# Performance work log

Hardware: AMD Instinct MI355X
Metric: run time of the kernel (lower is better)

The kernel has to match this reference:

```python
import jax, jax.numpy as jnp
import numpy as np

N = 50000   # nodes
E = 800000  # edges (avg degree 16)
F = 128     # n_input
H = 8       # n_heads
C = 16      # n_hidden (per-head out channels)
D = H * C   # 128


def setup_inputs() -> dict:
    key = jax.random.key(0)
    ks = jax.random.split(key, 12)
    s = lambda k, shape: (jax.random.normal(k, shape, dtype=jnp.float32) * 0.05)
    return {
        'x': jax.random.normal(ks[0], (N, F), dtype=jnp.float32),
        'edge_index': jax.random.randint(ks[1], (2, E), 0, N, dtype=jnp.int32),
        # GATv2Conv params (PyG defaults: share_weights=False, bias=True, neg_slope=0.2, self-loops)
        'W_l': s(ks[2], (F, D)),
        'b_l': jnp.zeros((D,), jnp.float32),
        'W_r': s(ks[3], (F, D)),
        'b_r': jnp.zeros((D,), jnp.float32),
        'att': s(ks[4], (H, C)),
        'conv_bias': jnp.zeros((D,), jnp.float32),
        # BatchNorm1d affine params
        'bn_gamma': jnp.ones((D,), jnp.float32),
        'bn_beta': jnp.zeros((D,), jnp.float32),
        # encoder output Linear
        'lin_W': s(ks[5], (D, D)),
        'lin_b': jnp.zeros((D,), jnp.float32),
        # EdgeDecoder scalars a, b (init 1.0)
        'a_edge': jnp.ones((1,), jnp.float32),
        'b_edge': jnp.ones((1,), jnp.float32),
        # LinearDecoder
        'dec2_W': s(ks[6], (D, F)),
        'dec2_b': jnp.zeros((F,), jnp.float32),
    }


def reference(x, edge_index, W_l, b_l, W_r, b_r, att, conv_bias,
              bn_gamma, bn_beta, lin_W, lin_b, a_edge, b_edge, dec2_W, dec2_b):
    n = x.shape[0]
    # GATv2Conv adds self-loops by default
    loop = jnp.arange(n, dtype=edge_index.dtype)
    src = jnp.concatenate([edge_index[0], loop])  # source j (messages come from)
    dst = jnp.concatenate([edge_index[1], loop])  # target i (softmax segments)
    xl = (x @ W_l + b_l).reshape(n, H, C)  # source transform
    xr = (x @ W_r + b_r).reshape(n, H, C)  # target transform
    # attention logits: a^T LeakyReLU(xl_j + xr_i), per head
    e = jax.nn.leaky_relu(xl[src] + xr[dst], negative_slope=0.2)  # [Et,H,C]
    logits = jnp.einsum('ehc,hc->eh', e, att)                     # [Et,H]
    # segment softmax over incoming edges of each target node
    m = jax.ops.segment_max(logits, dst, num_segments=n)
    ex = jnp.exp(logits - m[dst])
    denom = jax.ops.segment_sum(ex, dst, num_segments=n)
    alpha = ex / (denom[dst] + 1e-16)                             # [Et,H]
    # scatter-sum weighted source features, concat heads, add bias
    out = jax.ops.segment_sum(alpha[:, :, None] * xl[src], dst, num_segments=n)
    Hfeat = jax.nn.relu(out.reshape(n, D) + conv_bias)
    # BatchNorm1d, training-mode batch statistics (biased var), eps=1e-5
    mean = Hfeat.mean(axis=0)
    var = Hfeat.var(axis=0)
    Hn = (Hfeat - mean) / jnp.sqrt(var + 1e-5) * bn_gamma + bn_beta
    z = Hn @ lin_W + lin_b                                        # [N,D]
    # EdgeDecoder: gather + squared-diff + reduce over original edges
    dist = jnp.sum((z[edge_index[0]] - z[edge_index[1]]) ** 2, axis=1)  # [E]
    dist = jax.nn.relu(a_edge) * dist + b_edge
    value1 = jax.nn.sigmoid(-dist)                                # [E]
    # LinearDecoder
    value2 = z @ dec2_W + dec2_b                                  # [N,F]
    return (z, value1, value2)
```

## Files before the change

kernel.cpp:

```cpp
#include <hip/hip_runtime.h>

#define DD 128
#define HH 8
#define NBCOPY 32
#define PADS 4

typedef float f32x4 __attribute__((ext_vector_type(4)));
typedef short s16x8 __attribute__((ext_vector_type(8)));

__device__ __forceinline__ ushort f2b(float f) {
  unsigned u = __float_as_uint(f);
  unsigned r = u + 0x7fffu + ((u >> 16) & 1u);
  return (ushort)(r >> 16);
}
__device__ __forceinline__ float b2f(ushort b) {
  return __uint_as_float(((unsigned)b) << 16);
}
__device__ __forceinline__ void atomAddF(float* p, float v) {
#if defined(__HIP_DEVICE_COMPILE__)
  unsafeAtomicAdd(p, v);
#else
  atomicAdd(p, v);
#endif
}
__device__ __forceinline__ float lrelu(float v) { return fmaxf(v, 0.2f * v); }

__device__ __forceinline__ float sumC(const float* __restrict__ b8, int idx) {
  float s = 0.f;
#pragma unroll
  for (int c = 0; c < NBCOPY; c++) s += b8[(c << 8) + idx];
  return s;
}

__device__ __forceinline__ void packW_idx(int i, int& k, int& n) {
  int j = i & 7, l = (i >> 3) & 63, tile = i >> 9;
  int q = tile >> 3, c = tile & 7;
  k = q * 32 + ((l >> 4) << 3) + j;
  n = c * 16 + (l & 15);
}

__global__ __launch_bounds__(256) void k_prep(const float* __restrict__ x,
    ushort* __restrict__ xb, int total4, const float* __restrict__ Wl,
    const float* __restrict__ Wr, ushort* __restrict__ WlP,
    ushort* __restrict__ WrP, const int* __restrict__ ei,
    int* __restrict__ deg, int E, int convB, int packB) {
  int b = blockIdx.x;
  if (b < convB) {
    int i = b * 256 + threadIdx.x;
    if (i < total4) {
      float4 v = ((const float4*)x)[i];
      ushort4 o;
      o.x = f2b(v.x); o.y = f2b(v.y); o.z = f2b(v.z); o.w = f2b(v.w);
      ((ushort4*)xb)[i] = o;
    }
  } else if (b < convB + packB) {
    int t = (b - convB) * 256 + threadIdx.x;
    int side = t >> 14;
    int i = t & 16383;
    int k, n;
    packW_idx(i, k, n);
    if (side) WrP[i] = f2b(Wr[k * DD + n]);
    else      WlP[i] = f2b(Wl[k * DD + n]);
  } else {
    int e = (b - convB - packB) * 256 + threadIdx.x;
    if (e < E) atomicAdd(&deg[ei[E + e] << PADS], 1);
  }
}

__global__ __launch_bounds__(256) void k_part(const int* __restrict__ deg,
    int* __restrict__ rowstart, int* __restrict__ bsum, int N) {
  __shared__ int sc[256];
  int t = threadIdx.x;
  int i = blockIdx.x * 256 + t;
  int v = (i < N) ? deg[i << PADS] : 0;
  sc[t] = v;
  __syncthreads();
  for (int off = 1; off < 256; off <<= 1) {
    int u = (t >= off) ? sc[t - off] : 0;
    __syncthreads();
    sc[t] += u;
    __syncthreads();
  }
  if (i < N) rowstart[i] = sc[t] - v;
  if (t == 255) bsum[blockIdx.x] = sc[255];
}

__global__ __launch_bounds__(1024) void k_mid(const int* __restrict__ bsum,
    int* __restrict__ boff, int* __restrict__ rowstartN, int B) {
  __shared__ int sc[1024];
  int t = threadIdx.x;
  int v = (t < B) ? bsum[t] : 0;
  sc[t] = v;
  __syncthreads();
  for (int off = 1; off < 1024; off <<= 1) {
    int u = (t >= off) ? sc[t - off] : 0;
    __syncthreads();
    sc[t] += u;
    __syncthreads();
  }
  if (t < B) boff[t] = sc[t] - v;
  if (t == 1023) *rowstartN = sc[1023];
}

__global__ __launch_bounds__(256) void k_apply(int* __restrict__ rowstart,
    int* __restrict__ cursor, const int* __restrict__ boff, int N) {
  int i = blockIdx.x * 256 + threadIdx.x;
  if (i < N) {
    int r = rowstart[i] + boff[blockIdx.x];
    rowstart[i] = r;
    cursor[i << PADS] = r;
  }
}

__global__ __launch_bounds__(256) void k_lrfill(const ushort* __restrict__ xb,
    const ushort* __restrict__ WlP, const ushort* __restrict__ WrP,
    const float* __restrict__ bl, const float* __restrict__ br,
    ushort* __restrict__ xlb, ushort* __restrict__ xrb, int N, int mmB,
    const int* __restrict__ ei, int* __restrict__ cursor,
    int* __restrict__ csr_src, int E) {
  if ((int)blockIdx.x >= mmB) {
    int e = ((int)blockIdx.x - mmB) * 256 + threadIdx.x;
    if (e < E) {
      int d = ei[E + e];
      int pos = atomicAdd(&cursor[d << PADS], 1);
      csr_src[pos] = ei[e];
    }
    return;
  }
  int lane = threadIdx.x & 63;
  int wv = threadIdx.x >> 6;
  int rbase = blockIdx.x * 64 + wv * 16;
  int arow = rbase + (lane & 15);
  if (arow >= N) arow = 0;
  const ushort* ap = xb + (size_t)arow * DD + ((lane >> 4) << 3);
  s16x8 afr[4];
#pragma unroll
  for (int q = 0; q < 4; q++) afr[q] = *(const s16x8*)(ap + q * 32);
  const s16x8* BL = (const s16x8*)WlP;
  const s16x8* BR = (const s16x8*)WrP;
  f32x4 accL[8] = {}, accR[8] = {};
#pragma unroll
  for (int q = 0; q < 4; q++) {
#pragma unroll
    for (int c = 0; c < 8; c++) {
      accL[c] = __builtin_amdgcn_mfma_f32_16x16x32_bf16(
          afr[q], BL[(q * 8 + c) * 64 + lane], accL[c], 0, 0, 0);
      accR[c] = __builtin_amdgcn_mfma_f32_16x16x32_bf16(
          afr[q], BR[(q * 8 + c) * 64 + lane], accR[c], 0, 0, 0);
    }
  }
  int r0 = rbase + ((lane >> 4) << 2);
  int colb = lane & 15;
#pragma unroll
  for (int c = 0; c < 8; c++) {
    int col = c * 16 + colb;
    float vbl = bl[col], vbr = br[col];
#pragma unroll
    for (int r = 0; r < 4; r++) {
      int row = r0 + r;
      if (row < N) {
        xlb[(size_t)row * DD + col] = f2b(accL[c][r] + vbl);
        xrb[(size_t)row * DD + col] = f2b(accR[c][r] + vbr);
      }
    }
  }
}

__global__ __launch_bounds__(256) void k_agg(const ushort* __restrict__ xlb,
    const ushort* __restrict__ xrb, const int* __restrict__ rowstart,
    const int* __restrict__ csr_src, const float* __restrict__ att,
    const float* __restrict__ cb, ushort* __restrict__ hfb,
    float* __restrict__ bnsumC, int N) {
  int lane = threadIdx.x & 63;
  int wv = threadIdx.x >> 6;
  int d = (blockIdx.x * 256 + threadIdx.x) >> 6;
  bool active = d < N;
  int dc = active ? d : 0;
  float2 a = ((const float2*)att)[lane];
  float2 c = ((const float2*)cb)[lane];
  float vx = 0.f, vy = 0.f;
  {
    ushort2 rv = ((const ushort2*)(xrb + (size_t)dc * DD))[lane];
    float2 r = {b2f(rv.x), b2f(rv.y)};
    ushort2 gv = ((const ushort2*)(xlb + (size_t)dc * DD))[lane];
    float2 g0 = {b2f(gv.x), b2f(gv.y)};
    float t0 = lrelu(g0.x + r.x) * a.x + lrelu(g0.y + r.y) * a.y;
#pragma unroll
    for (int o = 4; o; o >>= 1) t0 += __shfl_xor(t0, o);
    float m0 = t0;
    float den0 = 1.f, den1 = 0.f, den2 = 0.f, den3 = 0.f;
    float2 acc0 = g0, acc1 = {0.f, 0.f}, acc2 = {0.f, 0.f}, acc3 = {0.f, 0.f};
    int i0 = rowstart[dc], i1 = active ? rowstart[dc + 1] : i0;
    int i = i0;
    for (; i + 4 <= i1; i += 4) {
      int s0 = csr_src[i], s1 = csr_src[i + 1];
      int s2 = csr_src[i + 2], s3 = csr_src[i + 3];
      ushort2 va = ((const ushort2*)(xlb + (size_t)s0 * DD))[lane];
      ushort2 vb = ((const ushort2*)(xlb + (size_t)s1 * DD))[lane];
      ushort2 vc = ((const ushort2*)(xlb + (size_t)s2 * DD))[lane];
      ushort2 vd = ((const ushort2*)(xlb + (size_t)s3 * DD))[lane];
      float2 ga = {b2f(va.x), b2f(va.y)};
      float2 gb = {b2f(vb.x), b2f(vb.y)};
      float2 gc = {b2f(vc.x), b2f(vc.y)};
      float2 gd = {b2f(vd.x), b2f(vd.y)};
      float ta = lrelu(ga.x + r.x) * a.x + lrelu(ga.y + r.y) * a.y;
      float tb = lrelu(gb.x + r.x) * a.x + lrelu(gb.y + r.y) * a.y;
      float tc = lrelu(gc.x + r.x) * a.x + lrelu(gc.y + r.y) * a.y;
      float td = lrelu(gd.x + r.x) * a.x + lrelu(gd.y + r.y) * a.y;
#pragma unroll
      for (int o = 4; o; o >>= 1) {
        ta += __shfl_xor(ta, o);
        tb += __shfl_xor(tb, o);
        tc += __shfl_xor(tc, o);
        td += __shfl_xor(td, o);
      }
      float ea = __expf(fminf(ta - m0, 60.f));
      float eb = __expf(fminf(tb - m0, 60.f));
      float ec = __expf(fminf(tc - m0, 60.f));
      float ed = __expf(fminf(td - m0, 60.f));
      den0 += ea; acc0.x += ea * ga.x; acc0.y += ea * ga.y;
      den1 += eb; acc1.x += eb * gb.x; acc1.y += eb * gb.y;
      den2 += ec; acc2.x += ec * gc.x; acc2.y += ec * gc.y;
      den3 += ed; acc3.x += ed * gd.x; acc3.y += ed * gd.y;
    }
    for (; i < i1; i++) {
      int s = csr_src[i];
      ushort2 va = ((const ushort2*)(xlb + (size_t)s * DD))[lane];
      float2 ga = {b2f(va.x), b2f(va.y)};
      float ta = lrelu(ga.x + r.x) * a.x + lrelu(ga.y + r.y) * a.y;
#pragma unroll
      for (int o = 4; o; o >>= 1) ta += __shfl_xor(ta, o);
      float ea = __expf(fminf(ta - m0, 60.f));
      den0 += ea;
      acc0.x += ea * ga.x;
      acc0.y += ea * ga.y;
    }
    float den = ((den0 + den1) + (den2 + den3)) + 1e-16f;
    float ax = (acc0.x + acc1.x) + (acc2.x + acc3.x);
    float ay = (acc0.y + acc1.y) + (acc2.y + acc3.y);
    float inv = 1.f / den;
    if (active) {
      vx = fmaxf(fmaf(ax, inv, c.x), 0.f);
      vy = fmaxf(fmaf(ay, inv, c.y), 0.f);
      ushort2 o2;
      o2.x = f2b(vx);
      o2.y = f2b(vy);
      ((ushort2*)(hfb + (size_t)dc * DD))[lane] = o2;
    }
  }
  __shared__ float4 red[4][64];
  red[wv][lane] = make_float4(vx, vx * vx, vy, vy * vy);
  __syncthreads();
  if (wv == 0) {
    float4 p0 = red[0][lane], p1 = red[1][lane];
    float4 p2 = red[2][lane], p3 = red[3][lane];
    float* bs = bnsumC + ((blockIdx.x & (NBCOPY - 1)) << 8);
    atomAddF(&bs[2 * lane],           (p0.x + p1.x) + (p2.x + p3.x));
    atomAddF(&bs[2 * lane + 1],       (p0.z + p1.z) + (p2.z + p3.z));
    atomAddF(&bs[DD + 2 * lane],      (p0.y + p1.y) + (p2.y + p3.y));
    atomAddF(&bs[DD + 2 * lane + 1],  (p0.w + p1.w) + (p2.w + p3.w));
  }
}

__global__ __launch_bounds__(256) void k_fold(const float* __restrict__ bnsumC,
    const float* __restrict__ gamma, const float* __restrict__ beta,
    const float* __restrict__ linW, const float* __restrict__ linb,
    const float* __restrict__ dec2W, const float* __restrict__ dec2b,
    float* __restrict__ b1p, float* __restrict__ b2pp,
    ushort* __restrict__ W1P, ushort* __restrict__ W2P, int N) {
  int b = blockIdx.x;
  float invN = 1.f / (float)N;
  if (b == 0) {
    int t = threadIdx.x;
    __shared__ float sshift[DD], sb1[DD];
    if (t < DD) {
      float mean = sumC(bnsumC, t) * invN;
      float var = sumC(bnsumC, DD + t) * invN - mean * mean;
      float sc = gamma[t] / sqrtf(var + 1e-5f);
      sshift[t] = beta[t] - mean * sc;
    }
    __syncthreads();
    if (t < DD) {
      float b1 = linb[t];
#pragma unroll 8
      for (int k = 0; k < DD; k++) b1 += sshift[k] * linW[k * DD + t];
      b1p[t] = b1;
      sb1[t] = b1;
    }
    __syncthreads();
    if (t < DD) {
      float b2v = dec2b[t];
#pragma unroll 8
      for (int k = 0; k < DD; k++) b2v += sb1[k] * dec2W[k * DD + t];
      b2pp[t] = b2v;
    }
  } else if (b <= 64) {
    int i = (b - 1) * 256 + threadIdx.x;
    int k, n;
    packW_idx(i, k, n);
    float mean = sumC(bnsumC, k) * invN;
    float var = sumC(bnsumC, DD + k) * invN - mean * mean;
    float sc = gamma[k] / sqrtf(var + 1e-5f);
    float s = 0.f;
#pragma unroll 8
    for (int kk = 0; kk < DD; kk++) s += linW[k * DD + kk] * dec2W[kk * DD + n];
    W2P[i] = f2b(sc * s);
  } else {
    int i = (b - 65) * 256 + threadIdx.x;
    int k, n;
    packW_idx(i, k, n);
    float mean = sumC(bnsumC, k) * invN;
    float var = sumC(bnsumC, DD + k) * invN - mean * mean;
    float sc = gamma[k] / sqrtf(var + 1e-5f);
    W1P[i] = f2b(sc * linW[k * DD + n]);
  }
}

__global__ __launch_bounds__(256) void k_mmz1(const ushort* __restrict__ hfb,
    const ushort* __restrict__ W1P, const float* __restrict__ b1p,
    float* __restrict__ z, ushort* __restrict__ zb, int N) {
  int lane = threadIdx.x & 63;
  int wv = threadIdx.x >> 6;
  int rbase = blockIdx.x * 64 + wv * 16;
  int arow = rbase + (lane & 15);
  if (arow >= N) arow = 0;
  const ushort* ap = hfb + (size_t)arow * DD + ((lane >> 4) << 3);
  s16x8 afr[4];
#pragma unroll
  for (int q = 0; q < 4; q++) afr[q] = *(const s16x8*)(ap + q * 32);
  const s16x8* B1 = (const s16x8*)W1P;
  f32x4 acc1[8] = {};
#pragma unroll
  for (int q = 0; q < 4; q++) {
#pragma unroll
    for (int c = 0; c < 8; c++) {
      acc1[c] = __builtin_amdgcn_mfma_f32_16x16x32_bf16(
          afr[q], B1[(q * 8 + c) * 64 + lane], acc1[c], 0, 0, 0);
    }
  }
  int r0 = rbase + ((lane >> 4) << 2);
  int colb = lane & 15;
#pragma unroll
  for (int c = 0; c < 8; c++) {
    int col = c * 16 + colb;
    float vb1 = b1p[col];
#pragma unroll
    for (int r = 0; r < 4; r++) {
      int row = r0 + r;
      if (row < N) {
        float zv = acc1[c][r] + vb1;
        z[(size_t)row * DD + col] = zv;
        zb[(size_t)row * DD + col] = f2b(zv);
      }
    }
  }
}

__global__ __launch_bounds__(256) void k_v2edge(const ushort* __restrict__ hfb,
    const ushort* __restrict__ W2P, const float* __restrict__ b2pp,
    float* __restrict__ v2, int N, int v2B,
    const ushort* __restrict__ zb, const int* __restrict__ ei,
    const float* __restrict__ ae, const float* __restrict__ be,
    float* __restrict__ v1, int E, int edgeB) {
  if ((int)blockIdx.x < v2B) {
    int lane = threadIdx.x & 63;
    int wv = threadIdx.x >> 6;
    int rbase = blockIdx.x * 64 + wv * 16;
    int arow = rbase + (lane & 15);
    if (arow >= N) arow = 0;
    const ushort* ap = hfb + (size_t)arow * DD + ((lane >> 4) << 3);
    s16x8 afr[4];
#pragma unroll
    for (int q = 0; q < 4; q++) afr[q] = *(const s16x8*)(ap + q * 32);
    const s16x8* B2 = (const s16x8*)W2P;
    f32x4 acc2[8] = {};
#pragma unroll
    for (int q = 0; q < 4; q++) {
#pragma unroll
      for (int c = 0; c < 8; c++) {
        acc2[c] = __builtin_amdgcn_mfma_f32_16x16x32_bf16(
            afr[q], B2[(q * 8 + c) * 64 + lane], acc2[c], 0, 0, 0);
      }
    }
    int r0 = rbase + ((lane >> 4) << 2);
    int colb = lane & 15;
#pragma unroll
    for (int c = 0; c < 8; c++) {
      int col = c * 16 + colb;
      float vb2 = b2pp[col];
#pragma unroll
      for (int r = 0; r < 4; r++) {
        int row = r0 + r;
        if (row < N) v2[(size_t)row * DD + col] = acc2[c][r] + vb2;
      }
    }
    return;
  }
  int lane = threadIdx.x & 63;
  int sub = lane >> 4;
  int cl = lane & 15;
  int wid = (((int)blockIdx.x - v2B) * 256 + threadIdx.x) >> 6;
  int nw = (edgeB * 256) >> 6;
  int nq = (E + 3) >> 2;
  float a = fmaxf(ae[0], 0.f), b = be[0];
  for (int q = wid; q < nq; q += nw) {
    int e = q * 4 + sub;
    bool ok = e < E;
    int ec = ok ? e : 0;
    int s = ei[ec], d = ei[E + ec];
    uint4 zs = *(const uint4*)(zb + (size_t)s * DD + cl * 8);
    uint4 zd = *(const uint4*)(zb + (size_t)d * DD + cl * 8);
    float v = 0.f;
    float dl, dh;
    dl = __uint_as_float(zs.x << 16) - __uint_as_float(zd.x << 16);
    dh = __uint_as_float(zs.x & 0xffff0000u) - __uint_as_float(zd.x & 0xffff0000u);
    v += dl * dl + dh * dh;
    dl = __uint_as_float(zs.y << 16) - __uint_as_float(zd.y << 16);
    dh = __uint_as_float(zs.y & 0xffff0000u) - __uint_as_float(zd.y & 0xffff0000u);
    v += dl * dl + dh * dh;
    dl = __uint_as_float(zs.z << 16) - __uint_as_float(zd.z << 16);
    dh = __uint_as_float(zs.z & 0xffff0000u) - __uint_as_float(zd.z & 0xffff0000u);
    v += dl * dl + dh * dh;
    dl = __uint_as_float(zs.w << 16) - __uint_as_float(zd.w << 16);
    dh = __uint_as_float(zs.w & 0xffff0000u) - __uint_as_float(zd.w & 0xffff0000u);
    v += dl * dl + dh * dh;
#pragma unroll
    for (int o = 8; o; o >>= 1) v += __shfl_xor(v, o);
    if (cl == 0 && ok) v1[e] = 1.f / (1.f + __expf(fmaf(a, v, b)));
  }
}

extern "C" void kernel_launch(void* const* d_in, const int* in_sizes, int n_in,
                              void* d_out, int out_size, void* d_ws, size_t ws_size,
                              hipStream_t stream) {
  const float* x = (const float*)d_in[0];
  const int* ei = (const int*)d_in[1];
  const float* Wl = (const float*)d_in[2];
  const float* bl = (const float*)d_in[3];
  const float* Wr = (const float*)d_in[4];
  const float* br = (const float*)d_in[5];
  const float* att = (const float*)d_in[6];
  const float* cb = (const float*)d_in[7];
  const float* gamma = (const float*)d_in[8];
  const float* beta = (const float*)d_in[9];
  const float* linW = (const float*)d_in[10];
  const float* linb = (const float*)d_in[11];
  const float* ae = (const float*)d_in[12];
  const float* be = (const float*)d_in[13];
  const float* dec2W = (const float*)d_in[14];
  const float* dec2b = (const float*)d_in[15];

  int N = in_sizes[0] / DD;
  int E = in_sizes[1] / 2;
  size_t ND = (size_t)N * DD;
  int B = (N + 255) / 256;

  char* wsb = (char*)d_ws;
  size_t o = 0;
  auto alloc = [&](size_t bytes) {
    void* p = wsb + o;
    o += (bytes + 15) & ~(size_t)15;
    return p;
  };
  ushort* xb  = (ushort*)alloc(ND * 2);
  ushort* xlb = (ushort*)alloc(ND * 2);
  ushort* xrb = (ushort*)alloc(ND * 2);
  ushort* hfb = (ushort*)alloc(ND * 2);
  ushort* zbb = (ushort*)alloc(ND * 2);
  ushort* WlP = (ushort*)alloc(DD * DD * 2);
  ushort* WrP = (ushort*)alloc(DD * DD * 2);
  ushort* W1P = (ushort*)alloc(DD * DD * 2);
  ushort* W2P = (ushort*)alloc(DD * DD * 2);
  float* b1p   = (float*)alloc(DD * 4);
  float* b2pp  = (float*)alloc(DD * 4);
  int* deg       = (int*)alloc(((size_t)N << PADS) * 4 + 64);
  float* bnsumC  = (float*)alloc(NBCOPY * 2 * DD * 4);
  size_t clearBytes = (char*)(bnsumC + NBCOPY * 2 * DD) - (char*)deg;
  int* rowstart = (int*)alloc((size_t)(N + 1) * 4);
  int* cursor   = (int*)alloc(((size_t)N << PADS) * 4 + 64);
  int* bsum     = (int*)alloc((size_t)B * 4);
  int* boff     = (int*)alloc((size_t)B * 4);
  int* csr_src  = (int*)alloc((size_t)E * 4);

  float* z = (float*)d_out;
  float* v1 = z + ND;
  float* v2 = v1 + E;

  hipMemsetAsync(deg, 0, clearBytes, stream);

  int total4 = (int)(ND / 4);
  int convB = (total4 + 255) / 256;
  int packB = 128;
  int degB = (E + 255) / 256;
  k_prep<<<convB + packB + degB, 256, 0, stream>>>(x, xb, total4, Wl, Wr, WlP,
                                                   WrP, ei, deg, E, convB, packB);
  k_part<<<B, 256, 0, stream>>>(deg, rowstart, bsum, N);
  k_mid<<<1, 1024, 0, stream>>>(bsum, boff, rowstart + N, B);
  k_apply<<<B, 256, 0, stream>>>(rowstart, cursor, boff, N);
  int mmB = (N + 63) / 64;
  int fillB = (E + 255) / 256;
  k_lrfill<<<mmB + fillB, 256, 0, stream>>>(xb, WlP, WrP, bl, br, xlb, xrb, N,
                                            mmB, ei, cursor, csr_src, E);
  k_agg<<<(N + 3) / 4, 256, 0, stream>>>(xlb, xrb, rowstart, csr_src, att, cb,
                                         hfb, bnsumC, N);
  k_fold<<<129, 256, 0, stream>>>(bnsumC, gamma, beta, linW, linb, dec2W,
                                  dec2b, b1p, b2pp, W1P, W2P, N);
  k_mmz1<<<(N + 63) / 64, 256, 0, stream>>>(hfb, W1P, b1p, z, zbb, N);
  int v2B = (N + 63) / 64;
  int edgeB = 2048;
  k_v2edge<<<v2B + edgeB, 256, 0, stream>>>(hfb, W2P, b2pp, v2, N, v2B, zbb,
                                            ei, ae, be, v1, E, edgeB);
}
```

Measured before the change: 241.9 us.

## Compute edge decoder per destination node via CSR, reusing destination z row

The edge decoder now walks the existing CSR (grouped by destination) with one wavefront per node. Each wave loads the destination z row once and reuses it for all incoming edges, so only source rows are gathered per edge. To scatter results back to the original edge order, the CSR fill also writes an edge-id array, which costs an extra E-sized write and read. Output writes to v1 become scattered, and load balance now follows node degree.

```diff
diff --git a/kernel.cpp b/kernel.cpp
--- a/kernel.cpp
+++ b/kernel.cpp
@@ -117,13 +117,14 @@
     const float* __restrict__ bl, const float* __restrict__ br,
     ushort* __restrict__ xlb, ushort* __restrict__ xrb, int N, int mmB,
     const int* __restrict__ ei, int* __restrict__ cursor,
-    int* __restrict__ csr_src, int E) {
+    int* __restrict__ csr_src, int* __restrict__ csr_eid, int E) {
   if ((int)blockIdx.x >= mmB) {
     int e = ((int)blockIdx.x - mmB) * 256 + threadIdx.x;
     if (e < E) {
       int d = ei[E + e];
       int pos = atomicAdd(&cursor[d << PADS], 1);
       csr_src[pos] = ei[e];
+      csr_eid[pos] = e;
     }
     return;
   }
@@ -359,9 +360,10 @@
 __global__ __launch_bounds__(256) void k_v2edge(const ushort* __restrict__ hfb,
     const ushort* __restrict__ W2P, const float* __restrict__ b2pp,
     float* __restrict__ v2, int N, int v2B,
-    const ushort* __restrict__ zb, const int* __restrict__ ei,
+    const ushort* __restrict__ zb, const int* __restrict__ rowstart,
+    const int* __restrict__ csr_src, const int* __restrict__ csr_eid,
     const float* __restrict__ ae, const float* __restrict__ be,
-    float* __restrict__ v1, int E, int edgeB) {
+    float* __restrict__ v1) {
   if ((int)blockIdx.x < v2B) {
     int lane = threadIdx.x & 63;
     int wv = threadIdx.x >> 6;
@@ -399,34 +401,38 @@
   int lane = threadIdx.x & 63;
   int sub = lane >> 4;
   int cl = lane & 15;
-  int wid = (((int)blockIdx.x - v2B) * 256 + threadIdx.x) >> 6;
-  int nw = (edgeB * 256) >> 6;
-  int nq = (E + 3) >> 2;
+  int d = ((((int)blockIdx.x - v2B) * 256) + threadIdx.x) >> 6;
+  if (d >= N) return;
   float a = fmaxf(ae[0], 0.f), b = be[0];
-  for (int q = wid; q < nq; q += nw) {
-    int e = q * 4 + sub;
-    bool ok = e < E;
-    int ec = ok ? e : 0;
-    int s = ei[ec], d = ei[E + ec];
+  uint4 zdv = *(const uint4*)(zb + (size_t)d * DD + cl * 8);
+  float dz0 = __uint_as_float(zdv.x << 16);
+  float dz1 = __uint_as_float(zdv.x & 0xffff0000u);
+  float dz2 = __uint_as_float(zdv.y << 16);
+  float dz3 = __uint_as_float(zdv.y & 0xffff0000u);
+  float dz4 = __uint_as_float(zdv.z << 16);
+  float dz5 = __uint_as_float(zdv.z & 0xffff0000u);
+  float dz6 = __uint_as_float(zdv.w << 16);
+  float dz7 = __uint_as_float(zdv.w & 0xffff0000u);
+  int i0 = rowstart[d], i1 = rowstart[d + 1];
+  for (int i = i0; i < i1; i += 4) {
+    int idx = i + sub;
+    bool ok = idx < i1;
+    int ic = ok ? idx : i0;
+    int s = csr_src[ic];
+    int eid = csr_eid[ic];
     uint4 zs = *(const uint4*)(zb + (size_t)s * DD + cl * 8);
-    uint4 zd = *(const uint4*)(zb + (size_t)d * DD + cl * 8);
-    float v = 0.f;
-    float dl, dh;
-    dl = __uint_as_float(zs.x << 16) - __uint_as_float(zd.x << 16);
-    dh = __uint_as_float(zs.x & 0xffff0000u) - __uint_as_float(zd.x & 0xffff0000u);
-    v += dl * dl + dh * dh;
-    dl = __uint_as_float(zs.y << 16) - __uint_as_float(zd.y << 16);
-    dh = __uint_as_float(zs.y & 0xffff0000u) - __uint_as_float(zd.y & 0xffff0000u);
-    v += dl * dl + dh * dh;
-    dl = __uint_as_float(zs.z << 16) - __uint_as_float(zd.z << 16);
-    dh = __uint_as_float(zs.z & 0xffff0000u) - __uint_as_float(zd.z & 0xffff0000u);
-    v += dl * dl + dh * dh;
-    dl = __uint_as_float(zs.w << 16) - __uint_as_float(zd.w << 16);
-    dh = __uint_as_float(zs.w & 0xffff0000u) - __uint_as_float(zd.w & 0xffff0000u);
-    v += dl * dl + dh * dh;
+    float t, v;
+    t = __uint_as_float(zs.x << 16) - dz0;          v  = t * t;
+    t = __uint_as_float(zs.x & 0xffff0000u) - dz1;  v += t * t;
+    t = __uint_as_float(zs.y << 16) - dz2;          v += t * t;
+    t = __uint_as_float(zs.y & 0xffff0000u) - dz3;  v += t * t;
+    t = __uint_as_float(zs.z << 16) - dz4;          v += t * t;
+    t = __uint_as_float(zs.z & 0xffff0000u) - dz5;  v += t * t;
+    t = __uint_as_float(zs.w << 16) - dz6;          v += t * t;
+    t = __uint_as_float(zs.w & 0xffff0000u) - dz7;  v += t * t;
 #pragma unroll
     for (int o = 8; o; o >>= 1) v += __shfl_xor(v, o);
-    if (cl == 0 && ok) v1[e] = 1.f / (1.f + __expf(fmaf(a, v, b)));
+    if (cl == 0 && ok) v1[eid] = 1.f / (1.f + __expf(fmaf(a, v, b)));
   }
 }
 
@@ -481,6 +487,7 @@
   int* bsum     = (int*)alloc((size_t)B * 4);
   int* boff     = (int*)alloc((size_t)B * 4);
   int* csr_src  = (int*)alloc((size_t)E * 4);
+  int* csr_eid  = (int*)alloc((size_t)E * 4);
 
   float* z = (float*)d_out;
   float* v1 = z + ND;
@@ -500,14 +507,15 @@
   int mmB = (N + 63) / 64;
   int fillB = (E + 255) / 256;
   k_lrfill<<<mmB + fillB, 256, 0, stream>>>(xb, WlP, WrP, bl, br, xlb, xrb, N,
-                                            mmB, ei, cursor, csr_src, E);
+                                            mmB, ei, cursor, csr_src, csr_eid, E);
   k_agg<<<(N + 3) / 4, 256, 0, stream>>>(xlb, xrb, rowstart, csr_src, att, cb,
                                          hfb, bnsumC, N);
   k_fold<<<129, 256, 0, stream>>>(bnsumC, gamma, beta, linW, linb, dec2W,
                                   dec2b, b1p, b2pp, W1P, W2P, N);
   k_mmz1<<<(N + 63) / 64, 256, 0, stream>>>(hfb, W1P, b1p, z, zbb, N);
   int v2B = (N + 63) / 64;
-  int edgeB = 2048;
+  int edgeB = (N + 3) / 4;
   k_v2edge<<<v2B + edgeB, 256, 0, stream>>>(hfb, W2P, b2pp, v2, N, v2B, zbb,
-                                            ei, ae, be, v1, E, edgeB);
-}
+                                            rowstart, csr_src, csr_eid, ae, be,
+                                            v1);
+}
```

Result: slower. 260.4 us (+7.6%).

## Process decoder edges in CSR (dst-sorted) order and remap results back

Applied to the files above, without the earlier changes.

The CSR fill now stores (src,dst) pairs and records each edge's CSR position. The edge decoder walks edges in dst-sorted order, so the z[dst] gathers hit consecutive rows and get cache reuse. A new remap kernel then scatters the per-edge sigmoid values back to their original order. This costs an extra kernel launch, wider CSR entries in the aggregation loads, and extra E-sized buffers for writing and reading.

```diff
diff --git a/kernel.cpp b/kernel.cpp
--- a/kernel.cpp
+++ b/kernel.cpp
@@ -117,13 +117,14 @@
     const float* __restrict__ bl, const float* __restrict__ br,
     ushort* __restrict__ xlb, ushort* __restrict__ xrb, int N, int mmB,
     const int* __restrict__ ei, int* __restrict__ cursor,
-    int* __restrict__ csr_src, int E) {
+    int2* __restrict__ csr_sd, int* __restrict__ pose, int E) {
   if ((int)blockIdx.x >= mmB) {
     int e = ((int)blockIdx.x - mmB) * 256 + threadIdx.x;
     if (e < E) {
       int d = ei[E + e];
       int pos = atomicAdd(&cursor[d << PADS], 1);
-      csr_src[pos] = ei[e];
+      csr_sd[pos] = make_int2(ei[e], d);
+      pose[e] = pos;
     }
     return;
   }
@@ -168,7 +169,7 @@
 
 __global__ __launch_bounds__(256) void k_agg(const ushort* __restrict__ xlb,
     const ushort* __restrict__ xrb, const int* __restrict__ rowstart,
-    const int* __restrict__ csr_src, const float* __restrict__ att,
+    const int2* __restrict__ csr_sd, const float* __restrict__ att,
     const float* __restrict__ cb, ushort* __restrict__ hfb,
     float* __restrict__ bnsumC, int N) {
   int lane = threadIdx.x & 63;
@@ -193,12 +194,12 @@
     int i0 = rowstart[dc], i1 = active ? rowstart[dc + 1] : i0;
     int i = i0;
     for (; i + 4 <= i1; i += 4) {
-      int s0 = csr_src[i], s1 = csr_src[i + 1];
-      int s2 = csr_src[i + 2], s3 = csr_src[i + 3];
-      ushort2 va = ((const ushort2*)(xlb + (size_t)s0 * DD))[lane];
-      ushort2 vb = ((const ushort2*)(xlb + (size_t)s1 * DD))[lane];
-      ushort2 vc = ((const ushort2*)(xlb + (size_t)s2 * DD))[lane];
-      ushort2 vd = ((const ushort2*)(xlb + (size_t)s3 * DD))[lane];
+      int2 sd0 = csr_sd[i], sd1 = csr_sd[i + 1];
+      int2 sd2 = csr_sd[i + 2], sd3 = csr_sd[i + 3];
+      ushort2 va = ((const ushort2*)(xlb + (size_t)sd0.x * DD))[lane];
+      ushort2 vb = ((const ushort2*)(xlb + (size_t)sd1.x * DD))[lane];
+      ushort2 vc = ((const ushort2*)(xlb + (size_t)sd2.x * DD))[lane];
+      ushort2 vd = ((const ushort2*)(xlb + (size_t)sd3.x * DD))[lane];
       float2 ga = {b2f(va.x), b2f(va.y)};
       float2 gb = {b2f(vb.x), b2f(vb.y)};
       float2 gc = {b2f(vc.x), b2f(vc.y)};
@@ -224,7 +225,7 @@
       den3 += ed; acc3.x += ed * gd.x; acc3.y += ed * gd.y;
     }
     for (; i < i1; i++) {
-      int s = csr_src[i];
+      int s = csr_sd[i].x;
       ushort2 va = ((const ushort2*)(xlb + (size_t)s * DD))[lane];
       float2 ga = {b2f(va.x), b2f(va.y)};
       float ta = lrelu(ga.x + r.x) * a.x + lrelu(ga.y + r.y) * a.y;
@@ -359,9 +360,9 @@
 __global__ __launch_bounds__(256) void k_v2edge(const ushort* __restrict__ hfb,
     const ushort* __restrict__ W2P, const float* __restrict__ b2pp,
     float* __restrict__ v2, int N, int v2B,
-    const ushort* __restrict__ zb, const int* __restrict__ ei,
+    const ushort* __restrict__ zb, const int2* __restrict__ csr_sd,
     const float* __restrict__ ae, const float* __restrict__ be,
-    float* __restrict__ v1, int E, int edgeB) {
+    float* __restrict__ v1c, int E, int edgeB) {
   if ((int)blockIdx.x < v2B) {
     int lane = threadIdx.x & 63;
     int wv = threadIdx.x >> 6;
@@ -404,30 +405,31 @@
   int nq = (E + 3) >> 2;
   float a = fmaxf(ae[0], 0.f), b = be[0];
   for (int q = wid; q < nq; q += nw) {
-    int e = q * 4 + sub;
-    bool ok = e < E;
-    int ec = ok ? e : 0;
-    int s = ei[ec], d = ei[E + ec];
-    uint4 zs = *(const uint4*)(zb + (size_t)s * DD + cl * 8);
-    uint4 zd = *(const uint4*)(zb + (size_t)d * DD + cl * 8);
-    float v = 0.f;
-    float dl, dh;
-    dl = __uint_as_float(zs.x << 16) - __uint_as_float(zd.x << 16);
-    dh = __uint_as_float(zs.x & 0xffff0000u) - __uint_as_float(zd.x & 0xffff0000u);
-    v += dl * dl + dh * dh;
-    dl = __uint_as_float(zs.y << 16) - __uint_as_float(zd.y << 16);
-    dh = __uint_as_float(zs.y & 0xffff0000u) - __uint_as_float(zd.y & 0xffff0000u);
-    v += dl * dl + dh * dh;
-    dl = __uint_as_float(zs.z << 16) - __uint_as_float(zd.z << 16);
-    dh = __uint_as_float(zs.z & 0xffff0000u) - __uint_as_float(zd.z & 0xffff0000u);
-    v += dl * dl + dh * dh;
-    dl = __uint_as_float(zs.w << 16) - __uint_as_float(zd.w << 16);
-    dh = __uint_as_float(zs.w & 0xffff0000u) - __uint_as_float(zd.w & 0xffff0000u);
-    v += dl * dl + dh * dh;
+    int p = q * 4 + sub;
+    bool ok = p < E;
+    int pc = ok ? p : 0;
+    int2 sd = csr_sd[pc];
+    uint4 zs = *(const uint4*)(zb + (size_t)sd.x * DD + cl * 8);
+    uint4 zd = *(const uint4*)(zb + (size_t)sd.y * DD + cl * 8);
+    float t, v;
+    t = __uint_as_float(zs.x << 16) - __uint_as_float(zd.x << 16);                  v  = t * t;
+    t = __uint_as_float(zs.x & 0xffff0000u) - __uint_as_float(zd.x & 0xffff0000u);  v += t * t;
+    t = __uint_as_float(zs.y << 16) - __uint_as_float(zd.y << 16);                  v += t * t;
+    t = __uint_as_float(zs.y & 0xffff0000u) - __uint_as_float(zd.y & 0xffff0000u);  v += t * t;
+    t = __uint_as_float(zs.z << 16) - __uint_as_float(zd.z << 16);                  v += t * t;
+    t = __uint_as_float(zs.z & 0xffff0000u) - __uint_as_float(zd.z & 0xffff0000u);  v += t * t;
+    t = __uint_as_float(zs.w << 16) - __uint_as_float(zd.w << 16);                  v += t * t;
+    t = __uint_as_float(zs.w & 0xffff0000u) - __uint_as_float(zd.w & 0xffff0000u);  v += t * t;
 #pragma unroll
     for (int o = 8; o; o >>= 1) v += __shfl_xor(v, o);
-    if (cl == 0 && ok) v1[e] = 1.f / (1.f + __expf(fmaf(a, v, b)));
-  }
+    if (cl == 0 && ok) v1c[p] = 1.f / (1.f + __expf(fmaf(a, v, b)));
+  }
+}
+
+__global__ __launch_bounds__(256) void k_remap(const float* __restrict__ v1c,
+    const int* __restrict__ pose, float* __restrict__ v1, int E) {
+  int e = blockIdx.x * 256 + threadIdx.x;
+  if (e < E) v1[e] = v1c[pose[e]];
 }
 
 extern "C" void kernel_launch(void* const* d_in, const int* in_sizes, int n_in,
@@ -480,7 +482,9 @@
   int* cursor   = (int*)alloc(((size_t)N << PADS) * 4 + 64);
   int* bsum     = (int*)alloc((size_t)B * 4);
   int* boff     = (int*)alloc((size_t)B * 4);
-  int* csr_src  = (int*)alloc((size_t)E * 4);
+  int2* csr_sd  = (int2*)alloc((size_t)E * 8);
+  int* pose     = (int*)alloc((size_t)E * 4);
+  float* v1c    = (float*)alloc((size_t)E * 4);
 
   float* z = (float*)d_out;
   float* v1 = z + ND;
@@ -500,8 +504,8 @@
   int mmB = (N + 63) / 64;
   int fillB = (E + 255) / 256;
   k_lrfill<<<mmB + fillB, 256, 0, stream>>>(xb, WlP, WrP, bl, br, xlb, xrb, N,
-                                            mmB, ei, cursor, csr_src, E);
-  k_agg<<<(N + 3) / 4, 256, 0, stream>>>(xlb, xrb, rowstart, csr_src, att, cb,
+                                            mmB, ei, cursor, csr_sd, pose, E);
+  k_agg<<<(N + 3) / 4, 256, 0, stream>>>(xlb, xrb, rowstart, csr_sd, att, cb,
                                          hfb, bnsumC, N);
   k_fold<<<129, 256, 0, stream>>>(bnsumC, gamma, beta, linW, linb, dec2W,
                                   dec2b, b1p, b2pp, W1P, W2P, N);
@@ -509,5 +513,6 @@
   int v2B = (N + 63) / 64;
   int edgeB = 2048;
   k_v2edge<<<v2B + edgeB, 256, 0, stream>>>(hfb, W2P, b2pp, v2, N, v2B, zbb,
-                                            ei, ae, be, v1, E, edgeB);
-}
+                                            csr_sd, ae, be, v1c, E, edgeB);
+  k_remap<<<(E + 255) / 256, 256, 0, stream>>>(v1c, pose, v1, E);
+}
```

New measurement: 245.8 us. Within noise of the previous version (+1.6%).
